# Optimization experiments

Hardware: AMD Instinct MI355X
Metric: run time of the kernel (lower is better)

Reference implementation:

```python
import jax, jax.numpy as jnp
import numpy as np

KH = KW = 3
K = KH * KW
PAD = 1


def conv3x3(x, w, b):
    # x: [B,C,H,W], w: [O,C,3,3], b: [O]
    y = jax.lax.conv_general_dilated(x, w, (1, 1), ((PAD, PAD), (PAD, PAD)),
                                     dimension_numbers=('NCHW', 'OIHW', 'NCHW'))
    return y + b[None, :, None, None]


def deform_conv(x, offsets, w, b):
    # torchvision DeformConv2d, stride=1, pad=1, dilation=1, groups=1, offset_groups=1
    # x: [B,C,H,W], offsets: [B,2*K,H,W] ordered (dy,dx) per kernel point, w: [O,C,3,3]
    B, C, H, W = x.shape
    O = w.shape[0]
    off = offsets.reshape(B, K, 2, H, W)
    dy, dx = off[:, :, 0], off[:, :, 1]                      # [B,K,H,W]
    kyy, kxx = jnp.meshgrid(jnp.arange(KH), jnp.arange(KW), indexing='ij')
    ky = kyy.reshape(K).astype(x.dtype)
    kx = kxx.reshape(K).astype(x.dtype)
    py = dy + ky[None, :, None, None] + jnp.arange(H, dtype=x.dtype)[None, None, :, None] - PAD
    px = dx + kx[None, :, None, None] + jnp.arange(W, dtype=x.dtype)[None, None, None, :] - PAD
    y0 = jnp.floor(py)
    x0 = jnp.floor(px)
    wy = (py - y0)[:, None]                                   # [B,1,K,H,W]
    wx = (px - x0)[:, None]
    y0i = y0.astype(jnp.int32)
    x0i = x0.astype(jnp.int32)
    xf = x.reshape(B, C, H * W)

    def gather(yi, xi):
        valid = (yi >= 0) & (yi < H) & (xi >= 0) & (xi < W)   # zero outside
        yc = jnp.clip(yi, 0, H - 1)
        xc = jnp.clip(xi, 0, W - 1)
        idx = (yc * W + xc).reshape(B, 1, K * H * W)
        g = jnp.take_along_axis(xf, idx, axis=2).reshape(B, C, K, H, W)
        return g * valid[:, None].astype(x.dtype)

    v00 = gather(y0i, x0i)
    v01 = gather(y0i, x0i + 1)
    v10 = gather(y0i + 1, x0i)
    v11 = gather(y0i + 1, x0i + 1)
    samp = (v00 * (1 - wy) * (1 - wx) + v01 * (1 - wy) * wx
            + v10 * wy * (1 - wx) + v11 * wy * wx)            # [B,C,K,H,W]
    out = jnp.einsum('bckhw,ock->bohw', samp, w.reshape(O, C, K))
    return out + b[None, :, None, None]


def deform_align(x, y, wo, bo, wd, bd):
    return deform_conv(x, conv3x3(y, wo, bo), wd, bd)


def setup_inputs() -> dict:
    key = jax.random.key(0)
    ks = jax.random.split(key, 16)
    inC, embedC = 64, 96
    B, H, W = 4, 96, 96
    s = 0.02
    d = {
        'x1': jax.random.normal(ks[0], (B, inC, H, W), jnp.float32),
        'y': jax.random.normal(ks[1], (B, inC, H, W), jnp.float32),
        # block 1: offset conv inC->2K, deform conv inC->embedC
        'wo1': jax.random.normal(ks[2], (2 * K, inC, 3, 3), jnp.float32) * s,
        'bo1': jnp.zeros((2 * K,), jnp.float32),
        'wd1': jax.random.normal(ks[3], (embedC, inC, 3, 3), jnp.float32) * s,
        'bd1': jnp.zeros((embedC,), jnp.float32),
        # block 2: embedC->2K, embedC->embedC
        'wo2': jax.random.normal(ks[4], (2 * K, embedC, 3, 3), jnp.float32) * s,
        'bo2': jnp.zeros((2 * K,), jnp.float32),
        'wd2': jax.random.normal(ks[5], (embedC, embedC, 3, 3), jnp.float32) * s,
        'bd2': jnp.zeros((embedC,), jnp.float32),
        # block 3: embedC->2K, embedC->inC
        'wo3': jax.random.normal(ks[6], (2 * K, embedC, 3, 3), jnp.float32) * s,
        'bo3': jnp.zeros((2 * K,), jnp.float32),
        'wd3': jax.random.normal(ks[7], (inC, embedC, 3, 3), jnp.float32) * s,
        'bd3': jnp.zeros((inC,), jnp.float32),
    }
    return d


def reference(x1, y, wo1, bo1, wd1, bd1, wo2, bo2, wd2, bd2, wo3, bo3, wd3, bd3):
    h = deform_align(x1, y, wo1, bo1, wd1, bd1)
    h = deform_align(h, h, wo2, bo2, wd2, bd2)
    h = deform_align(h, h, wo3, bo3, wd3, bd3)
    return h
```

## Files before the change

### kernel.cpp

```cpp
#include <hip/hip_runtime.h>

constexpr int B = 4, H = 96, W = 96, HW = H * W;
constexpr int NPIX = B * HW;
constexpr int KOFF = 18;

typedef _Float16 half8 __attribute__((ext_vector_type(8)));
typedef _Float16 half4 __attribute__((ext_vector_type(4)));
typedef float f32x4 __attribute__((ext_vector_type(4)));
typedef __attribute__((address_space(3))) _Float16 lf16;

__device__ __forceinline__ int iclamp(int v, int lo, int hi) {
  return v < lo ? lo : (v > hi ? hi : v);
}

struct Corners {
  int i00, i01, i10, i11;
  float w00, w01, w10, w11;
};

__device__ __forceinline__ Corners mk_corners(float py, float qx) {
  float fy = floorf(py), fx = floorf(qx);
  float wy = py - fy, wx = qx - fx;
  int y0 = (int)fy, x0 = (int)fx;
  int y1 = y0 + 1, x1 = x0 + 1;
  bool vy0 = (y0 >= 0) & (y0 < H);
  bool vy1 = (y1 >= 0) & (y1 < H);
  bool vx0 = (x0 >= 0) & (x0 < W);
  bool vx1 = (x1 >= 0) & (x1 < W);
  int r0 = iclamp(y0, 0, H - 1) * W;
  int r1 = iclamp(y1, 0, H - 1) * W;
  int c0 = iclamp(x0, 0, W - 1);
  int c1 = iclamp(x1, 0, W - 1);
  Corners cc;
  cc.i00 = r0 + c0; cc.i01 = r0 + c1; cc.i10 = r1 + c0; cc.i11 = r1 + c1;
  float a = 1.f - wy, bb = 1.f - wx;
  cc.w00 = a * bb * ((vy0 & vx0) ? 1.f : 0.f);
  cc.w01 = a * wx * ((vy0 & vx1) ? 1.f : 0.f);
  cc.w10 = wy * bb * ((vy1 & vx0) ? 1.f : 0.f);
  cc.w11 = wy * wx * ((vy1 & vx1) ? 1.f : 0.f);
  return cc;
}

__device__ __forceinline__ void gld_lds16(const _Float16* g, lf16* l) {
  __builtin_amdgcn_global_load_lds(
      (const __attribute__((address_space(1))) void*)g,
      (__attribute__((address_space(3))) void*)l, 16, 0, 0);
}

template <int NF>
__device__ __forceinline__ void stage_coop(const _Float16* wk, lf16* lb, int lane,
                                           int wid) {
#pragma unroll
  for (int i = 0; i < (NF + 3) / 4; ++i) {
    int f = i * 4 + wid;
    if (f < NF)
      gld_lds16(wk + (size_t)f * 512 + lane * 8, lb + f * 512);
  }
}

template <int KS>
__device__ __forceinline__ void load_corners(const _Float16* xb, int ch, const Corners& cc,
                                             half8 r[KS][4]) {
  const _Float16* p00 = xb + (size_t)cc.i00 * (KS * 32) + ch;
  const _Float16* p01 = xb + (size_t)cc.i01 * (KS * 32) + ch;
  const _Float16* p10 = xb + (size_t)cc.i10 * (KS * 32) + ch;
  const _Float16* p11 = xb + (size_t)cc.i11 * (KS * 32) + ch;
#pragma unroll
  for (int ks = 0; ks < KS; ++ks) {
    r[ks][0] = *(const half8*)(p00 + ks * 32);
    r[ks][1] = *(const half8*)(p01 + ks * 32);
    r[ks][2] = *(const half8*)(p10 + ks * 32);
    r[ks][3] = *(const half8*)(p11 + ks * 32);
  }
}

template <int KS>
__device__ __forceinline__ void interp_corners(const Corners& cc, half8 r[KS][4],
                                               half8 a[KS]) {
  _Float16 q00 = (_Float16)cc.w00, q01 = (_Float16)cc.w01;
  _Float16 q10 = (_Float16)cc.w10, q11 = (_Float16)cc.w11;
#pragma unroll
  for (int ks = 0; ks < KS; ++ks)
    a[ks] = r[ks][0] * q00 + r[ks][1] * q01 + r[ks][2] * q10 + r[ks][3] * q11;
}

template <int KS>
__device__ __forceinline__ void load_shift(const _Float16* xb, int ch, int h, int w,
                                           int ky, int kx, half8 a[KS]) {
  int yy = h + ky, xx = w + kx;
  bool v = (yy >= 0) & (yy < H) & (xx >= 0) & (xx < W);
  int yc = iclamp(yy, 0, H - 1), xc = iclamp(xx, 0, W - 1);
  const _Float16* pv = xb + (size_t)(yc * W + xc) * (KS * 32) + ch;
#pragma unroll
  for (int ks = 0; ks < KS; ++ks) {
    half8 r = *(const half8*)(pv + ks * 32);
    half8 z = {0, 0, 0, 0, 0, 0, 0, 0};
    a[ks] = v ? r : z;
  }
}

template <int KS, int NJ, int J0, int J1>
__device__ __forceinline__ void mfma_dual(const _Float16* lb, int lane,
                                          half8 a0[KS], half8 a1[KS],
                                          f32x4 acc0[NJ], f32x4 acc1[NJ]) {
#pragma unroll
  for (int ks = 0; ks < KS; ++ks)
#pragma unroll
    for (int j = J0; j < J1; ++j) {
      half8 b = *(const half8*)(lb + (ks * NJ + j) * 512 + lane * 8);
      acc0[j] = __builtin_amdgcn_mfma_f32_16x16x32_f16(a0[ks], b, acc0[j], 0, 0, 0);
      acc1[j] = __builtin_amdgcn_mfma_f32_16x16x32_f16(a1[ks], b, acc1[j], 0, 0, 0);
    }
}

struct WAll {
  const float* src[6];
  _Float16* dst[6];
  int C[6], Osrc[6], OPAD[6], base[6];
};

__global__ void wfrag_all_kernel(WAll wa) {
  int bid = blockIdx.x;
  int s = 0;
#pragma unroll
  for (int i = 1; i < 6; ++i) s += (bid >= wa.base[i]) ? 1 : 0;
  int fid = bid - wa.base[s];
  int C = wa.C[s], Osrc = wa.Osrc[s], OPAD = wa.OPAD[s];
  const float* wsrc = wa.src[s];
  _Float16* wf = wa.dst[s];
  int KS = C / 32;
  int NJ = OPAD / 16;
  int lane = threadIdx.x;
  int j = fid % NJ;
  int ks = (fid / NJ) % KS;
  int k = fid / (NJ * KS);
  int o = j * 16 + (lane & 15);
  int c0 = ks * 32 + (lane >> 4) * 8;
  half8 v;
#pragma unroll
  for (int u = 0; u < 8; ++u)
    v[u] = (o < Osrc) ? (_Float16)wsrc[((size_t)o * C + c0 + u) * 9 + k] : (_Float16)0.f;
  *(half8*)(wf + ((size_t)fid * 64 + lane) * 8) = v;
}

__global__ __launch_bounds__(256) void repack2_kernel(const float* __restrict__ in0,
                                                      const float* __restrict__ in1,
                                                      _Float16* __restrict__ o0,
                                                      _Float16* __restrict__ o1) {
  constexpr int C = 64;
  const float* in = blockIdx.y ? in1 : in0;
  _Float16* outh = blockIdx.y ? o1 : o0;
  __shared__ float tile[64 * C];
  int t = threadIdx.x;
  int pix0 = blockIdx.x * 64;
  int b = pix0 / HW;
  int hw0 = pix0 - b * HW;
  int l = t & 63;
  for (int cc = t >> 6; cc < C; cc += 4)
    tile[cc * 64 + l] = in[((size_t)b * C + cc) * HW + hw0 + l];
  __syncthreads();
  int pl = t >> 2;
  int cq = t & 3;
  _Float16* op = outh + (size_t)(pix0 + pl) * C + cq * (C / 4);
#pragma unroll
  for (int c = 0; c < C / 4; c += 4) {
    half4 hv;
#pragma unroll
    for (int u = 0; u < 4; ++u) hv[u] = (_Float16)tile[(cq * (C / 4) + c + u) * 64 + pl];
    *(half4*)(op + c) = hv;
  }
}

template <int C, int O, bool WF32, bool WH>
__global__ __launch_bounds__(256, 1)
void stage_kernel(const _Float16* __restrict__ xoff, const _Float16* __restrict__ xdef,
                  const _Float16* __restrict__ wfo, const float* __restrict__ bo,
                  const _Float16* __restrict__ wfd, const float* __restrict__ bd,
                  float* __restrict__ out, _Float16* __restrict__ outh) {
  constexpr int KS = C / 32;
  constexpr int NJ = O / 16;
  constexpr int NFD = KS * NJ;
  constexpr int NFO = KS * 2;
  __shared__ _Float16 ldsB[2 * NFD * 512];
  __shared__ float lofs[128][KOFF];
  lf16* lb3 = (lf16*)ldsB;
  const int tid = threadIdx.x;
  const int wid = tid >> 6;
  const int lane = tid & 63;
  const int row = lane & 15;
  const int kgrp = lane >> 4;
  const int ch = kgrp * 8;
  const int chunk = (blockIdx.x & 7) * (int)(gridDim.x >> 3) + (blockIdx.x >> 3);
  const int px0 = chunk * 128 + wid * 32;
  const int b = px0 / HW;
  const int hw0 = px0 - b * HW;
  const int hwm0 = hw0 + row, hwm1 = hw0 + 16 + row;
  const int h0 = hwm0 / W, w0 = hwm0 - h0 * W;
  const int h1 = hwm1 / W, w1 = hwm1 - h1 * W;
  const _Float16* xo = xoff + (size_t)b * HW * C;
  const _Float16* xd = xdef + (size_t)b * HW * C;

  {
    f32x4 aoc0[2], aoc1[2];
#pragma unroll
    for (int j = 0; j < 2; ++j) {
      int o = j * 16 + row;
      float bv = (o < KOFF) ? bo[o] : 0.f;
      aoc0[j] = {bv, bv, bv, bv};
      aoc1[j] = {bv, bv, bv, bv};
    }
    half8 a0[KS], a1[KS], n0[KS], n1[KS];
    stage_coop<NFO>(wfo, lb3, lane, wid);
    load_shift<KS>(xo, ch, h0, w0, -1, -1, a0);
    load_shift<KS>(xo, ch, h1, w1, -1, -1, a1);
#pragma unroll
    for (int k = 0; k < 9; ++k) {
      __syncthreads();
      if (k < 8) {
        int kn = k + 1;
        stage_coop<NFO>(wfo + (size_t)kn * (NFO * 512),
                        lb3 + (kn & 1) * NFD * 512, lane, wid);
        load_shift<KS>(xo, ch, h0, w0, kn / 3 - 1, kn % 3 - 1, n0);
        load_shift<KS>(xo, ch, h1, w1, kn / 3 - 1, kn % 3 - 1, n1);
      }
      mfma_dual<KS, 2, 0, 2>(ldsB + (k & 1) * NFD * 512, lane, a0, a1, aoc0, aoc1);
      if (k < 8) {
#pragma unroll
        for (int ks = 0; ks < KS; ++ks) { a0[ks] = n0[ks]; a1[ks] = n1[ks]; }
      }
    }
#pragma unroll
    for (int j = 0; j < 2; ++j) {
      int o = j * 16 + row;
      if (o < KOFF) {
#pragma unroll
        for (int r = 0; r < 4; ++r) {
          lofs[wid * 32 + kgrp * 4 + r][o] = aoc0[j][r];
          lofs[wid * 32 + 16 + kgrp * 4 + r][o] = aoc1[j][r];
        }
      }
    }
  }
  __syncthreads();

  const int prow0 = wid * 32 + row, prow1 = prow0 + 16;
  const float hf0 = (float)(h0 - 1), wf0_ = (float)(w0 - 1);
  const float hf1 = (float)(h1 - 1), wf1_ = (float)(w1 - 1);

  f32x4 acc0[NJ], acc1[NJ];
#pragma unroll
  for (int j = 0; j < NJ; ++j) {
    float bv = bd[j * 16 + row];
    acc0[j] = {bv, bv, bv, bv};
    acc1[j] = {bv, bv, bv, bv};
  }
  half8 a0[KS], a1[KS], a0n[KS], a1n[KS];
  half8 rn[KS][4];
  stage_coop<NFD>(wfd, lb3, lane, wid);
  {
    Corners c0 = mk_corners(lofs[prow0][0] + hf0, lofs[prow0][1] + wf0_);
    load_corners<KS>(xd, ch, c0, rn);
    interp_corners<KS>(c0, rn, a0);
    Corners c1 = mk_corners(lofs[prow1][0] + hf1, lofs[prow1][1] + wf1_);
    load_corners<KS>(xd, ch, c1, rn);
    interp_corners<KS>(c1, rn, a1);
  }
#pragma unroll
  for (int k = 0; k < 9; ++k) {
    __syncthreads();
    const _Float16* lbk = ldsB + (k & 1) * NFD * 512;
    if (k < 8) {
      int kn = k + 1;
      stage_coop<NFD>(wfd + (size_t)kn * (NFD * 512),
                      lb3 + (kn & 1) * NFD * 512, lane, wid);
      float kyf = (float)(kn / 3), kxf = (float)(kn % 3);
      Corners cn0 = mk_corners(lofs[prow0][2 * kn] + hf0 + kyf,
                               lofs[prow0][2 * kn + 1] + wf0_ + kxf);
      load_corners<KS>(xd, ch, cn0, rn);
      mfma_dual<KS, NJ, 0, NJ / 2>(lbk, lane, a0, a1, acc0, acc1);
      interp_corners<KS>(cn0, rn, a0n);
      Corners cn1 = mk_corners(lofs[prow1][2 * kn] + hf1 + kyf,
                               lofs[prow1][2 * kn + 1] + wf1_ + kxf);
      load_corners<KS>(xd, ch, cn1, rn);
      mfma_dual<KS, NJ, NJ / 2, NJ>(lbk, lane, a0, a1, acc0, acc1);
      interp_corners<KS>(cn1, rn, a1n);
#pragma unroll
      for (int ks = 0; ks < KS; ++ks) { a0[ks] = a0n[ks]; a1[ks] = a1n[ks]; }
    } else {
      mfma_dual<KS, NJ, 0, NJ>(lbk, lane, a0, a1, acc0, acc1);
    }
  }
#pragma unroll
  for (int j = 0; j < NJ; ++j) {
    int o = j * 16 + row;
#pragma unroll
    for (int r2 = 0; r2 < 4; ++r2) {
      int p0 = px0 + kgrp * 4 + r2;
      int p1 = p0 + 16;
      if (WF32) {
        out[((size_t)b * O + o) * HW + (p0 - b * HW)] = acc0[j][r2];
        out[((size_t)b * O + o) * HW + (p1 - b * HW)] = acc1[j][r2];
      }
      if (WH) {
        outh[(size_t)p0 * O + o] = (_Float16)acc0[j][r2];
        outh[(size_t)p1 * O + o] = (_Float16)acc1[j][r2];
      }
    }
  }
}

extern "C" void kernel_launch(void* const* d_in, const int* in_sizes, int n_in,
                              void* d_out, int out_size, void* d_ws, size_t ws_size,
                              hipStream_t stream) {
  const float* x1  = (const float*)d_in[0];
  const float* y   = (const float*)d_in[1];
  const float* wo1 = (const float*)d_in[2];
  const float* bo1 = (const float*)d_in[3];
  const float* wd1 = (const float*)d_in[4];
  const float* bd1 = (const float*)d_in[5];
  const float* wo2 = (const float*)d_in[6];
  const float* bo2 = (const float*)d_in[7];
  const float* wd2 = (const float*)d_in[8];
  const float* bd2 = (const float*)d_in[9];
  const float* wo3 = (const float*)d_in[10];
  const float* bo3 = (const float*)d_in[11];
  const float* wd3 = (const float*)d_in[12];
  const float* bd3 = (const float*)d_in[13];
  float* out = (float*)d_out;

  char* p = (char*)d_ws;
  auto alloc = [&](size_t bytes) {
    char* r = p;
    p += (bytes + 255) & ~(size_t)255;
    return r;
  };
  _Float16* Wo1f = (_Float16*)alloc((size_t)9 * 2 * 2 * 512 * 2);
  _Float16* Wo2f = (_Float16*)alloc((size_t)9 * 3 * 2 * 512 * 2);
  _Float16* Wo3f = (_Float16*)alloc((size_t)9 * 3 * 2 * 512 * 2);
  _Float16* W1f  = (_Float16*)alloc((size_t)9 * 2 * 6 * 512 * 2);
  _Float16* W2f  = (_Float16*)alloc((size_t)9 * 3 * 6 * 512 * 2);
  _Float16* W3f  = (_Float16*)alloc((size_t)9 * 3 * 4 * 512 * 2);
  _Float16* x1h = (_Float16*)alloc((size_t)NPIX * 64 * 2);
  _Float16* yh  = (_Float16*)alloc((size_t)NPIX * 64 * 2);
  _Float16* h1h = (_Float16*)alloc((size_t)NPIX * 96 * 2);
  _Float16* h2h = (_Float16*)alloc((size_t)NPIX * 96 * 2);

  WAll wa;
  wa.src[0] = wo1; wa.dst[0] = Wo1f; wa.C[0] = 64; wa.Osrc[0] = 18; wa.OPAD[0] = 32;
  wa.src[1] = wo2; wa.dst[1] = Wo2f; wa.C[1] = 96; wa.Osrc[1] = 18; wa.OPAD[1] = 32;
  wa.src[2] = wo3; wa.dst[2] = Wo3f; wa.C[2] = 96; wa.Osrc[2] = 18; wa.OPAD[2] = 32;
  wa.src[3] = wd1; wa.dst[3] = W1f;  wa.C[3] = 64; wa.Osrc[3] = 96; wa.OPAD[3] = 96;
  wa.src[4] = wd2; wa.dst[4] = W2f;  wa.C[4] = 96; wa.Osrc[4] = 96; wa.OPAD[4] = 96;
  wa.src[5] = wd3; wa.dst[5] = W3f;  wa.C[5] = 96; wa.Osrc[5] = 64; wa.OPAD[5] = 64;
  int base = 0;
  for (int i = 0; i < 6; ++i) {
    wa.base[i] = base;
    base += 9 * (wa.C[i] / 32) * (wa.OPAD[i] / 16);
  }
  hipLaunchKernelGGL(wfrag_all_kernel, dim3(base), dim3(64), 0, stream, wa);
  hipLaunchKernelGGL(repack2_kernel, dim3(NPIX / 64, 2), dim3(256), 0, stream,
                     x1, y, x1h, yh);

  dim3 gs(NPIX / 128);
  dim3 wb(256);

  hipLaunchKernelGGL((stage_kernel<64, 96, false, true>), gs, wb, 0, stream,
                     yh, x1h, Wo1f, bo1, W1f, bd1, (float*)nullptr, h1h);
  hipLaunchKernelGGL((stage_kernel<96, 96, false, true>), gs, wb, 0, stream,
                     h1h, h1h, Wo2f, bo2, W2f, bd2, (float*)nullptr, h2h);
  hipLaunchKernelGGL((stage_kernel<96, 64, true, false>), gs, wb, 0, stream,
                     h2h, h2h, Wo3f, bo3, W3f, bd3, out, (_Float16*)nullptr);
}
```

Baseline: 151.6 us.

## Halve block size to 2 waves and batch offset-conv weight staging per chunk

Blocks now hold 2 waves covering 64 pixels instead of 4 waves covering 128, doubling the grid. The LDS weight staging loops are parameterized by wave count. The offset-conv phase stages several kernel taps' weights per barrier by packing them into the larger deform buffer, which cuts the number of __syncthreads from 9 to ceil(9/TPC). The aim is better CU occupancy and load balance with fewer barriers, at the cost of staging weights more often per pixel, since each block covers fewer pixels.

Measured after the change: 122.9 us. 19.0% less time.

```diff
diff --git a/kernel.cpp b/kernel.cpp
--- a/kernel.cpp
+++ b/kernel.cpp
@@ -47,14 +47,25 @@
       (__attribute__((address_space(3))) void*)l, 16, 0, 0);
 }
 
-template <int NF>
+template <int NF, int NW>
 __device__ __forceinline__ void stage_coop(const _Float16* wk, lf16* lb, int lane,
                                            int wid) {
 #pragma unroll
-  for (int i = 0; i < (NF + 3) / 4; ++i) {
-    int f = i * 4 + wid;
+  for (int i = 0; i < (NF + NW - 1) / NW; ++i) {
+    int f = i * NW + wid;
     if (f < NF)
       gld_lds16(wk + (size_t)f * 512 + lane * 8, lb + f * 512);
+  }
+}
+
+template <int NFO, int TPC, int NW>
+__device__ __forceinline__ void stage_chunk(const _Float16* w, lf16* lb, int lane,
+                                            int wid, int tstart) {
+#pragma unroll
+  for (int i = 0; i < (TPC * NFO + NW - 1) / NW; ++i) {
+    int f = i * NW + wid;
+    if (f < TPC * NFO && (tstart + f / NFO) < 9)
+      gld_lds16(w + ((size_t)tstart * NFO + f) * 512 + lane * 8, lb + f * 512);
   }
 }
 
@@ -172,7 +183,7 @@
 }
 
 template <int C, int O, bool WF32, bool WH>
-__global__ __launch_bounds__(256, 1)
+__global__ __launch_bounds__(128, 1)
 void stage_kernel(const _Float16* __restrict__ xoff, const _Float16* __restrict__ xdef,
                   const _Float16* __restrict__ wfo, const float* __restrict__ bo,
                   const _Float16* __restrict__ wfd, const float* __restrict__ bd,
@@ -181,8 +192,10 @@
   constexpr int NJ = O / 16;
   constexpr int NFD = KS * NJ;
   constexpr int NFO = KS * 2;
+  constexpr int TPC = NFD / NFO;
+  constexpr int NCH = (9 + TPC - 1) / TPC;
   __shared__ _Float16 ldsB[2 * NFD * 512];
-  __shared__ float lofs[128][KOFF];
+  __shared__ float lofs[64][KOFF];
   lf16* lb3 = (lf16*)ldsB;
   const int tid = threadIdx.x;
   const int wid = tid >> 6;
@@ -191,9 +204,9 @@
   const int kgrp = lane >> 4;
   const int ch = kgrp * 8;
   const int chunk = (blockIdx.x & 7) * (int)(gridDim.x >> 3) + (blockIdx.x >> 3);
-  const int px0 = chunk * 128 + wid * 32;
-  const int b = px0 / HW;
-  const int hw0 = px0 - b * HW;
+  const int pxw = chunk * 64 + wid * 32;
+  const int b = pxw / HW;
+  const int hw0 = pxw - b * HW;
   const int hwm0 = hw0 + row, hwm1 = hw0 + 16 + row;
   const int h0 = hwm0 / W, w0 = hwm0 - h0 * W;
   const int h1 = hwm1 / W, w1 = hwm1 - h1 * W;
@@ -210,23 +223,31 @@
       aoc1[j] = {bv, bv, bv, bv};
     }
     half8 a0[KS], a1[KS], n0[KS], n1[KS];
-    stage_coop<NFO>(wfo, lb3, lane, wid);
+    stage_chunk<NFO, TPC, 2>(wfo, lb3, lane, wid, 0);
     load_shift<KS>(xo, ch, h0, w0, -1, -1, a0);
     load_shift<KS>(xo, ch, h1, w1, -1, -1, a1);
 #pragma unroll
-    for (int k = 0; k < 9; ++k) {
+    for (int c = 0; c < NCH; ++c) {
       __syncthreads();
-      if (k < 8) {
-        int kn = k + 1;
-        stage_coop<NFO>(wfo + (size_t)kn * (NFO * 512),
-                        lb3 + (kn & 1) * NFD * 512, lane, wid);
-        load_shift<KS>(xo, ch, h0, w0, kn / 3 - 1, kn % 3 - 1, n0);
-        load_shift<KS>(xo, ch, h1, w1, kn / 3 - 1, kn % 3 - 1, n1);
-      }
-      mfma_dual<KS, 2, 0, 2>(ldsB + (k & 1) * NFD * 512, lane, a0, a1, aoc0, aoc1);
-      if (k < 8) {
-#pragma unroll
-        for (int ks = 0; ks < KS; ++ks) { a0[ks] = n0[ks]; a1[ks] = n1[ks]; }
+      if (c + 1 < NCH)
+        stage_chunk<NFO, TPC, 2>(wfo, lb3 + ((c + 1) & 1) * NFD * 512, lane, wid,
+                                 (c + 1) * TPC);
+      const _Float16* bufc = ldsB + (c & 1) * NFD * 512;
+#pragma unroll
+      for (int t = 0; t < TPC; ++t) {
+        int k = c * TPC + t;
+        if (k < 9) {
+          if (k < 8) {
+            int kn = k + 1;
+            load_shift<KS>(xo, ch, h0, w0, kn / 3 - 1, kn % 3 - 1, n0);
+            load_shift<KS>(xo, ch, h1, w1, kn / 3 - 1, kn % 3 - 1, n1);
+          }
+          mfma_dual<KS, 2, 0, 2>(bufc + t * NFO * 512, lane, a0, a1, aoc0, aoc1);
+          if (k < 8) {
+#pragma unroll
+            for (int ks = 0; ks < KS; ++ks) { a0[ks] = n0[ks]; a1[ks] = n1[ks]; }
+          }
+        }
       }
     }
 #pragma unroll
@@ -256,7 +277,7 @@
   }
   half8 a0[KS], a1[KS], a0n[KS], a1n[KS];
   half8 rn[KS][4];
-  stage_coop<NFD>(wfd, lb3, lane, wid);
+  stage_coop<NFD, 2>(wfd, lb3, lane, wid);
   {
     Corners c0 = mk_corners(lofs[prow0][0] + hf0, lofs[prow0][1] + wf0_);
     load_corners<KS>(xd, ch, c0, rn);
@@ -271,8 +292,8 @@
     const _Float16* lbk = ldsB + (k & 1) * NFD * 512;
     if (k < 8) {
       int kn = k + 1;
-      stage_coop<NFD>(wfd + (size_t)kn * (NFD * 512),
-                      lb3 + (kn & 1) * NFD * 512, lane, wid);
+      stage_coop<NFD, 2>(wfd + (size_t)kn * (NFD * 512),
+                         lb3 + (kn & 1) * NFD * 512, lane, wid);
       float kyf = (float)(kn / 3), kxf = (float)(kn % 3);
       Corners cn0 = mk_corners(lofs[prow0][2 * kn] + hf0 + kyf,
                                lofs[prow0][2 * kn + 1] + wf0_ + kxf);
@@ -295,7 +316,7 @@
     int o = j * 16 + row;
 #pragma unroll
     for (int r2 = 0; r2 < 4; ++r2) {
-      int p0 = px0 + kgrp * 4 + r2;
+      int p0 = pxw + kgrp * 4 + r2;
       int p1 = p0 + 16;
       if (WF32) {
         out[((size_t)b * O + o) * HW + (p0 - b * HW)] = acc0[j][r2];
@@ -361,8 +382,8 @@
   hipLaunchKernelGGL(repack2_kernel, dim3(NPIX / 64, 2), dim3(256), 0, stream,
                      x1, y, x1h, yh);
 
-  dim3 gs(NPIX / 128);
-  dim3 wb(256);
+  dim3 gs(NPIX / 64);
+  dim3 wb(128);
 
   hipLaunchKernelGGL((stage_kernel<64, 96, false, true>), gs, wb, 0, stream,
                      yh, x1h, Wo1f, bo1, W1f, bd1, (float*)nullptr, h1h);
```
